# Kernel optimization log

Measured on AMD Instinct MI355X. Metric: run time of the kernel, lower is better.

## Reference

```python
import jax, jax.numpy as jnp
import numpy as np

B, P, F, H, NF, E, V, L = 128, 196, 2048, 512, 512, 512, 10000, 20
T = L - 1
EPS = 1e-5  # BatchNorm eps (eval mode, running_mean=0, running_var=1)


def setup_inputs() -> dict:
    key = jax.random.key(0)
    ks = jax.random.split(key, 16)

    def kaiming(k, out_d, in_d):
        return jax.random.normal(k, (out_d, in_d), jnp.float32) * np.float32(np.sqrt(2.0 / in_d))

    encoder_feat = jax.random.normal(ks[0], (B, P, F), jnp.float32)
    gt_captions = jax.random.randint(ks[1], (B, L), 0, V)
    # lengths in [2, L], sorted descending (torch code assumes this), max forced to L
    captions_len = jnp.sort(jax.random.randint(ks[2], (B,), 2, L + 1))[::-1].at[0].set(L)

    emb = jax.random.uniform(ks[3], (V, E), jnp.float32, -0.1, 0.1)
    Wfa = kaiming(ks[4], NF, F); bfa = jnp.zeros((NF,), jnp.float32)
    Wha = kaiming(ks[5], NF, H); bha = jnp.zeros((NF,), jnp.float32)
    Wv = kaiming(ks[6], 1, NF); bv = jnp.zeros((1,), jnp.float32)
    Wh0 = kaiming(ks[7], H, F); bh0 = jnp.zeros((H,), jnp.float32)
    Wc0 = kaiming(ks[8], H, F); bc0 = jnp.zeros((H,), jnp.float32)
    gamma_h = jnp.ones((H,), jnp.float32); beta_h = jnp.zeros((H,), jnp.float32)
    gamma_c = jnp.ones((H,), jnp.float32); beta_c = jnp.zeros((H,), jnp.float32)
    Wfb = kaiming(ks[9], F, H); bfb = jnp.zeros((F,), jnp.float32)
    s = np.float32(1.0 / np.sqrt(H))  # torch LSTMCell default init range
    Wih = jax.random.uniform(ks[10], (4 * H, E + F), jnp.float32, -s, s)
    Whh = jax.random.uniform(ks[11], (4 * H, H), jnp.float32, -s, s)
    bih = jax.random.uniform(ks[12], (4 * H,), jnp.float32, -s, s)
    bhh = jax.random.uniform(ks[13], (4 * H,), jnp.float32, -s, s)
    Wfc = kaiming(ks[14], V, H); bfc = jnp.zeros((V,), jnp.float32)

    return dict(encoder_feat=encoder_feat, emb=emb, Wfa=Wfa, bfa=bfa, Wha=Wha, bha=bha,
                Wv=Wv, bv=bv, Wh0=Wh0, bh0=bh0, Wc0=Wc0, bc0=bc0,
                gamma_h=gamma_h, beta_h=beta_h, gamma_c=gamma_c, beta_c=beta_c,
                Wfb=Wfb, bfb=bfb, Wih=Wih, Whh=Whh, bih=bih, bhh=bhh,
                Wfc=Wfc, bfc=bfc, gt_captions=gt_captions, captions_len=captions_len)


def reference(encoder_feat, emb, Wfa, bfa, Wha, bha, Wv, bv, Wh0, bh0, Wc0, bc0,
              gamma_h, beta_h, gamma_c, beta_c, Wfb, bfb, Wih, Whh, bih, bhh,
              Wfc, bfc, gt_captions, captions_len):
    # Eval-mode semantics: dropout = identity, weight-drop inactive,
    # BatchNorm1d uses default running stats (mean=0, var=1).
    def bn(x, g, b):
        return g * (x / jnp.sqrt(1.0 + EPS)) + b

    feat = encoder_feat.mean(axis=1)                       # [B, F]
    h = bn(jax.nn.sigmoid(feat @ Wh0.T + bh0), gamma_h, beta_h)
    c = bn(jax.nn.sigmoid(feat @ Wc0.T + bc0), gamma_c, beta_c)

    # attention key projection is h-independent: hoist out of the time loop
    feat_att = jnp.einsum('bpf,nf->bpn', encoder_feat, Wfa) + bfa  # [B, P, NF]
    emb_seq = emb[gt_captions]                                      # [B, L, E]

    # ragged batch handled by masking (equivalent to torch's [:batch_size_t] slicing)
    mask = (jnp.arange(T)[:, None] < (captions_len - 1)[None, :]).astype(encoder_feat.dtype)  # [T, B]
    xs = (jnp.swapaxes(emb_seq[:, :T], 0, 1), mask)

    def step(carry, xt):
        h, c = carry
        emb_t, m = xt                                      # [B, E], [B]
        att = jax.nn.relu(feat_att + (h @ Wha.T + bha)[:, None, :])
        e = jnp.einsum('bpn,n->bp', att, Wv[0]) + bv[0]    # [B, P]
        alpha = jax.nn.softmax(e, axis=1)
        context = jnp.einsum('bpf,bp->bf', encoder_feat, alpha)
        gate = jax.nn.sigmoid(h @ Wfb.T + bfb)             # [B, F]
        x = jnp.concatenate([emb_t, gate * context], axis=1)
        gates = x @ Wih.T + bih + h @ Whh.T + bhh          # [B, 4H]
        i, f, g, o = jnp.split(gates, 4, axis=1)
        c_new = jax.nn.sigmoid(f) * c + jax.nn.sigmoid(i) * jnp.tanh(g)
        h_new = jax.nn.sigmoid(o) * jnp.tanh(c_new)
        preds = h_new @ Wfc.T + bfc                        # [B, V]
        mf = m[:, None]
        return (h_new, c_new), (preds * mf, alpha * mf)

    _, (preds, alphas) = jax.lax.scan(step, (h, c), xs)
    predictions = jnp.swapaxes(preds, 0, 1)                # [B, T, V]
    alphas = jnp.swapaxes(alphas, 0, 1)                    # [B, T, P]
    return predictions, alphas
```

## Files before the change

kernel.cpp:

```cpp
#include <hip/hip_runtime.h>
#include <cstdint>
#include <cstddef>

#define B_  128
#define P_  196
#define F_  2048
#define H_  512
#define NF_ 512
#define E_  512
#define V_  10000
#define L_  20
#define T_  19
#define NPAD_ 10112

typedef short s8v __attribute__((ext_vector_type(8)));
typedef float f32x4 __attribute__((ext_vector_type(4)));
typedef unsigned short u16x8 __attribute__((ext_vector_type(8)));

__device__ __forceinline__ float sigf(float x) { return 1.0f / (1.0f + expf(-x)); }
__device__ __forceinline__ ushort f2b(float f) {
    unsigned u = __builtin_bit_cast(unsigned, f);
    u += 0x7fff + ((u >> 16) & 1);
    return (ushort)(u >> 16);
}
__device__ __forceinline__ float b2f(ushort h) {
    unsigned u = ((unsigned)h) << 16;
    return __builtin_bit_cast(float, u);
}

__global__ __launch_bounds__(256)
void cast_mat(const float* __restrict__ s, ushort* __restrict__ d,
              long long total, int cols, int sld, int srows) {
    long long i4 = ((long long)blockIdx.x * 256 + threadIdx.x) * 4;
    if (i4 >= total) return;
    int n = (int)(i4 / cols);
    int k = (int)(i4 - (long long)n * cols);
    float4 v = make_float4(0.f, 0.f, 0.f, 0.f);
    if (n < srows) v = *(const float4*)(s + (size_t)n * sld + k);
    ushort4 o;
    o.x = f2b(v.x); o.y = f2b(v.y); o.z = f2b(v.z); o.w = f2b(v.w);
    *(ushort4*)(d + i4) = o;
}

__global__ __launch_bounds__(256)
void cast_perm(const float* __restrict__ s, ushort* __restrict__ d,
               int cols, int sld) {
    int idx = blockIdx.x * 256 + threadIdx.x;
    int i4 = idx * 4;
    int n = i4 / cols;
    int k = i4 - n * cols;
    int r = (n & 3) * H_ + (n >> 2);
    float4 v = *(const float4*)(s + (size_t)r * sld + k);
    ushort4 o;
    o.x = f2b(v.x); o.y = f2b(v.y); o.z = f2b(v.z); o.w = f2b(v.w);
    *(ushort4*)(d + (size_t)n * cols + k) = o;
}

__global__ __launch_bounds__(256)
void build_bg(const float* __restrict__ bih, const float* __restrict__ bhh,
              float* __restrict__ bg) {
    int n = blockIdx.x * 256 + threadIdx.x;
    int r = (n & 3) * H_ + (n >> 2);
    bg[n] = bih[r] + bhh[r];
}

#define NCP_ (2560 + NPAD_)
__global__ __launch_bounds__(256)
void build_bcp(const float* __restrict__ bha, const float* __restrict__ bfb,
               const float* __restrict__ bfc, float* __restrict__ bcp) {
    int n = blockIdx.x * 256 + threadIdx.x;
    if (n >= NCP_) return;
    float v;
    if (n < 512) v = bha[n];
    else if (n < 2560) v = bfb[n - 512];
    else { int r = n - 2560; v = (r < V_) ? bfc[r] : 0.0f; }
    bcp[n] = v;
}

__global__ __launch_bounds__(256)
void mean_cast_kernel(const float* __restrict__ enc, ushort* __restrict__ encb,
                      float* __restrict__ feat) {
    int b = blockIdx.x >> 3;
    int f = ((blockIdx.x & 7) << 8) + threadIdx.x;
    const float* p = enc + (size_t)b * P_ * F_ + f;
    ushort* pb = encb + (size_t)b * P_ * F_ + f;
    float s = 0.0f;
    for (int q = 0; q < P_; q++) {
        float v = p[(size_t)q * F_];
        pb[(size_t)q * F_] = f2b(v);
        s += v;
    }
    feat[b * F_ + f] = s * (1.0f / 196.0f);
}

__global__ __launch_bounds__(256) void mean_kernel(const float* __restrict__ enc,
                                                   float* __restrict__ feat) {
    int b = blockIdx.x >> 3;
    int f = ((blockIdx.x & 7) << 8) + threadIdx.x;
    const float* p = enc + (size_t)b * P_ * F_ + f;
    float s = 0.0f;
    for (int q = 0; q < P_; q++) s += p[(size_t)q * F_];
    feat[b * F_ + f] = s * (1.0f / 196.0f);
}

__global__ __launch_bounds__(256) void gather_b(const float* __restrict__ emb,
                                                const int* __restrict__ gt,
                                                ushort* __restrict__ embx) {
    int idx = blockIdx.x * 256 + threadIdx.x;
    int i4 = idx * 4;
    int e = i4 & (E_ - 1);
    int bt = i4 >> 9;
    int b = bt / T_, t = bt - b * T_;
    int tok = gt[b * L_ + t];
    float4 v = *(const float4*)(emb + (size_t)tok * E_ + e);
    ushort4 o;
    o.x = f2b(v.x); o.y = f2b(v.y); o.z = f2b(v.z); o.w = f2b(v.w);
    *(ushort4*)(embx + i4) = o;
}

__global__ __launch_bounds__(256)
void gemm_biasb(const float* __restrict__ A, int lda,
                const float* __restrict__ W, int ldw,
                const float* __restrict__ bias,
                ushort* __restrict__ C, long long ldc,
                int M, int N, int K) {
    __shared__ float As[16][65];
    __shared__ float Ws[16][65];
    const int tid = threadIdx.x;
    const int m0 = blockIdx.y << 6;
    const int n0 = blockIdx.x << 6;
    const int row = tid >> 2;
    const int kq  = (tid & 3) << 2;
    const int ty = tid >> 4, tx = tid & 15;
    float acc[4][4] = {};
    for (int k0 = 0; k0 < K; k0 += 16) {
        float4 av = make_float4(0.f, 0.f, 0.f, 0.f);
        float4 wv = make_float4(0.f, 0.f, 0.f, 0.f);
        int m = m0 + row;
        if (m < M) av = *(const float4*)(A + (size_t)m * lda + k0 + kq);
        int n = n0 + row;
        if (n < N) wv = *(const float4*)(W + (size_t)n * ldw + k0 + kq);
        __syncthreads();
        As[kq + 0][row] = av.x; As[kq + 1][row] = av.y;
        As[kq + 2][row] = av.z; As[kq + 3][row] = av.w;
        Ws[kq + 0][row] = wv.x; Ws[kq + 1][row] = wv.y;
        Ws[kq + 2][row] = wv.z; Ws[kq + 3][row] = wv.w;
        __syncthreads();
#pragma unroll
        for (int k = 0; k < 16; k++) {
            float a[4], w[4];
#pragma unroll
            for (int i = 0; i < 4; i++) a[i] = As[k][(ty << 2) + i];
#pragma unroll
            for (int j = 0; j < 4; j++) w[j] = Ws[k][(tx << 2) + j];
#pragma unroll
            for (int i = 0; i < 4; i++)
#pragma unroll
                for (int j = 0; j < 4; j++)
                    acc[i][j] = fmaf(a[i], w[j], acc[i][j]);
        }
    }
#pragma unroll
    for (int i = 0; i < 4; i++) {
        int m = m0 + (ty << 2) + i;
        if (m >= M) continue;
#pragma unroll
        for (int j = 0; j < 4; j++) {
            int n = n0 + (tx << 2) + j;
            if (n >= N) continue;
            C[(size_t)m * ldc + n] = f2b(acc[i][j] + bias[n]);
        }
    }
}

enum { MEPI_NONE = 0, MEPI_BIAS = 1, MEPI_BIASB = 2, MEPI_PREDS = 3 };

__device__ __forceinline__ void stage_tile(const ushort* __restrict__ g, int ld,
                                           int row0, int k0, ushort* lds,
                                           int rows, int w, int l) {
    int nchunk = rows >> 4;
    for (int c = w; c < nchunk; c += 4) {
        int flat = c * 1024 + l * 16;
        int r = flat >> 6;
        int ce = (flat & 63) >> 1;
        const ushort* gp = g + (size_t)(row0 + r) * ld + (k0 + ce);
        __builtin_amdgcn_global_load_lds(
            (const __attribute__((address_space(1))) void*)gp,
            (__attribute__((address_space(3))) void*)(lds + c * 512),
            16, 0, 0);
    }
}

template <int BM, int EPI, int DUAL, int SWZ = 0>
__global__ __launch_bounds__(256)
void mfma_gemm(const ushort* __restrict__ A1, int lda1,
               const ushort* __restrict__ W1, int ldw1, int K1,
               const ushort* __restrict__ A2, int lda2,
               const ushort* __restrict__ W2, int ldw2, int K2,
               const float* __restrict__ bias, void* __restrict__ Cout, long long ldc,
               void* __restrict__ Cout2,
               int M, int N,
               const int* __restrict__ clen, int tcur) {
    __shared__ ushort As[BM * 32];
    __shared__ ushort Bs[128 * 32];
    const int tid = threadIdx.x;
    const int w = tid >> 6, l = tid & 63;
    const int wr = w >> 1, wc = w & 1;
    constexpr int WM = BM / 2;
    constexpr int AF = WM / 16;
    int bx = blockIdx.x, by = blockIdx.y;
    if (SWZ) {
        const int gx = gridDim.x;
        const int nwg = gx * gridDim.y;
        const int fid = by * gx + bx;
        const int q = nwg >> 3, r = nwg & 7;
        const int xcd = fid & 7, idx = fid >> 3;
        const int nf = (xcd < r ? xcd * (q + 1)
                                : r * (q + 1) + (xcd - r) * q) + idx;
        bx = nf % gx; by = nf / gx;
    }
    const int m0 = by * BM;
    const int n0 = bx * 128;
    const int lrow = l & 15, lk8 = (l >> 4) * 8;
    const int kz = blockIdx.z, nzz = gridDim.z;

    f32x4 acc[AF][4] = {};

    for (int pass = 0; pass < 1 + DUAL; pass++) {
        const ushort* A = pass ? A2 : A1;
        const ushort* W = pass ? W2 : W1;
        const int lda = pass ? lda2 : lda1;
        const int ldw = pass ? ldw2 : ldw1;
        const int K  = pass ? K2 : K1;
        const int chunk = K / nzz;
        const int kbeg = kz * chunk;
        const int kend = kbeg + chunk;
        for (int k0 = kbeg; k0 < kend; k0 += 32) {
            __syncthreads();
            stage_tile(A, lda, m0, k0, As, BM, w, l);
            stage_tile(W, ldw, n0, k0, Bs, 128, w, l);
            __syncthreads();
            s8v af[AF], bf[4];
#pragma unroll
            for (int i = 0; i < AF; i++)
                af[i] = *(const s8v*)(As + (wr * WM + i * 16 + lrow) * 32 + lk8);
#pragma unroll
            for (int j = 0; j < 4; j++)
                bf[j] = *(const s8v*)(Bs + (wc * 64 + j * 16 + lrow) * 32 + lk8);
#pragma unroll
            for (int i = 0; i < AF; i++)
#pragma unroll
                for (int j = 0; j < 4; j++)
                    acc[i][j] = __builtin_amdgcn_mfma_f32_16x16x32_bf16(
                        af[i], bf[j], acc[i][j], 0, 0, 0);
        }
    }

    float* Cz = (float*)Cout + (size_t)kz * (size_t)M * ldc;
#pragma unroll
    for (int i = 0; i < AF; i++) {
        int rb = m0 + wr * WM + i * 16 + (l >> 4) * 4;
#pragma unroll
        for (int j = 0; j < 4; j++) {
            int n = n0 + wc * 64 + j * 16 + (l & 15);
            if (n >= N) continue;
#pragma unroll
            for (int r = 0; r < 4; r++) {
                int m = rb + r;
                float v = acc[i][j][r];
                if (EPI == MEPI_NONE) {
                    Cz[(size_t)m * ldc + n] = v;
                } else if (EPI == MEPI_BIAS) {
                    ((float*)Cout)[(size_t)m * ldc + n] = v + bias[n];
                } else if (EPI == MEPI_BIASB) {
                    ((ushort*)Cout)[(size_t)m * ldc + n] = f2b(v + bias[n]);
                } else if (EPI == MEPI_PREDS) {
                    if (n < V_) {
                        int bb = m & (B_ - 1);
                        int tt = m >> 7;
                        float mk = (tt < clen[bb] - 1) ? 1.0f : 0.0f;
                        ((float*)Cout)[((size_t)bb * T_ + tt) * (size_t)V_ + n] =
                            (v + bias[n]) * mk;
                    }
                }
            }
        }
    }
}

__global__ __launch_bounds__(256)
void h0c0_final(const float* __restrict__ part,
                const float* __restrict__ b0,
                const float* __restrict__ g0,
                const float* __restrict__ bt0,
                float* __restrict__ cbuf, ushort* __restrict__ hb) {
    int idx = blockIdx.x * 256 + threadIdx.x;
    int b = idx >> 9, j = idx & 511;
    const float rbn = 1.0f / sqrtf(1.0f + 1e-5f);
    float sh = b0[j], sc = b0[j + 512];
    for (int z = 0; z < 4; z++) {
        sh += part[((size_t)z * B_ + b) * 1024 + j];
        sc += part[((size_t)z * B_ + b) * 1024 + j + 512];
    }
    float hv = g0[j] * (sigf(sh) * rbn) + bt0[j];
    float cv = g0[j + 512] * (sigf(sc) * rbn) + bt0[j + 512];
    cbuf[idx] = cv;
    hb[idx] = f2b(hv);
}

template <int BF>
__global__ __launch_bounds__(256)
void attn_ctx(const void* __restrict__ encv, const ushort* __restrict__ fa,
              const float* __restrict__ combo, const float* __restrict__ Wv,
              float* __restrict__ alphas_out, const int* __restrict__ clen,
              ushort* __restrict__ gctxb, int t) {
    int b = blockIdx.x >> 1;
    int half = blockIdx.x & 1;
    int tid = threadIdx.x;
    int w = tid >> 6, l = tid & 63;
    __shared__ float eS[256];
    __shared__ float red[256];
    __shared__ float pc[128 * 8];
    const float* hap = combo + (size_t)b * 2560;
    float ha8[8], wv8[8];
#pragma unroll
    for (int i = 0; i < 8; i++) { ha8[i] = hap[l * 8 + i]; wv8[i] = Wv[l * 8 + i]; }
    eS[tid] = -1e30f;
    __syncthreads();
    const ushort* fab = fa + (size_t)b * P_ * NF_;
    for (int p = w; p < P_; p += 4) {
        const ushort* fp = fab + (size_t)p * NF_ + l * 8;
        ushort4 u0 = *(const ushort4*)fp;
        ushort4 u1 = *(const ushort4*)(fp + 4);
        float s = 0.0f, v;
        v = b2f(u0.x) + ha8[0]; v = v > 0.f ? v : 0.f; s = fmaf(v, wv8[0], s);
        v = b2f(u0.y) + ha8[1]; v = v > 0.f ? v : 0.f; s = fmaf(v, wv8[1], s);
        v = b2f(u0.z) + ha8[2]; v = v > 0.f ? v : 0.f; s = fmaf(v, wv8[2], s);
        v = b2f(u0.w) + ha8[3]; v = v > 0.f ? v : 0.f; s = fmaf(v, wv8[3], s);
        v = b2f(u1.x) + ha8[4]; v = v > 0.f ? v : 0.f; s = fmaf(v, wv8[4], s);
        v = b2f(u1.y) + ha8[5]; v = v > 0.f ? v : 0.f; s = fmaf(v, wv8[5], s);
        v = b2f(u1.z) + ha8[6]; v = v > 0.f ? v : 0.f; s = fmaf(v, wv8[6], s);
        v = b2f(u1.w) + ha8[7]; v = v > 0.f ? v : 0.f; s = fmaf(v, wv8[7], s);
#pragma unroll
        for (int off = 32; off > 0; off >>= 1) s += __shfl_down(s, off, 64);
        if (l == 0) eS[p] = s;
    }
    __syncthreads();
    float ev = eS[tid];
    red[tid] = ev;
    __syncthreads();
    for (int s = 128; s > 0; s >>= 1) {
        if (tid < s) red[tid] = fmaxf(red[tid], red[tid + s]);
        __syncthreads();
    }
    float mx = red[0];
    __syncthreads();
    float ex = expf(ev - mx);
    red[tid] = ex;
    __syncthreads();
    for (int s = 128; s > 0; s >>= 1) {
        if (tid < s) red[tid] += red[tid + s];
        __syncthreads();
    }
    float inv = 1.0f / red[0];
    float a = ex * inv;
    __syncthreads();
    eS[tid] = a;
    if (half == 0 && tid < P_) {
        float m = (t < clen[b] - 1) ? 1.0f : 0.0f;
        alphas_out[((size_t)b * T_ + t) * P_ + tid] = a * m;
    }
    __syncthreads();

    int tl = tid & 127;
    int pr = tid >> 7;
    int pp0 = pr * 98;
    int f0 = (half << 10) + tl * 8;
    float s[8] = {};
    if (BF) {
        const ushort* ep = (const ushort*)encv + (size_t)b * P_ * F_ +
                           (size_t)pp0 * F_ + f0;
        for (int p = 0; p < 98; p++) {
            u16x8 u = *(const u16x8*)(ep + (size_t)p * F_);
            float al = eS[pp0 + p];
#pragma unroll
            for (int i = 0; i < 8; i++) s[i] = fmaf(al, b2f(u[i]), s[i]);
        }
    } else {
        const float* ep = (const float*)encv + (size_t)b * P_ * F_ +
                          (size_t)pp0 * F_ + f0;
        for (int p = 0; p < 98; p++) {
            float4 u0 = *(const float4*)(ep + (size_t)p * F_);
            float4 u1 = *(const float4*)(ep + (size_t)p * F_ + 4);
            float al = eS[pp0 + p];
            s[0] = fmaf(al, u0.x, s[0]); s[1] = fmaf(al, u0.y, s[1]);
            s[2] = fmaf(al, u0.z, s[2]); s[3] = fmaf(al, u0.w, s[3]);
            s[4] = fmaf(al, u1.x, s[4]); s[5] = fmaf(al, u1.y, s[5]);
            s[6] = fmaf(al, u1.z, s[6]); s[7] = fmaf(al, u1.w, s[7]);
        }
    }
    if (pr) {
#pragma unroll
        for (int i = 0; i < 8; i++) pc[tl * 8 + i] = s[i];
    }
    __syncthreads();
    if (!pr) {
        const float* gp = combo + (size_t)b * 2560 + 512 + f0;
        float4 ga = *(const float4*)gp;
        float4 gb = *(const float4*)(gp + 4);
        float gv[8] = {ga.x, ga.y, ga.z, ga.w, gb.x, gb.y, gb.z, gb.w};
        ushort o[8];
#pragma unroll
        for (int i = 0; i < 8; i++)
            o[i] = f2b(sigf(gv[i]) * (s[i] + pc[tl * 8 + i]));
        *(u16x8*)(gctxb + (size_t)b * F_ + f0) = *(u16x8*)o;
    }
}

__global__ __launch_bounds__(256)
void lstm_perm(const float* __restrict__ gatesP,
               const float* __restrict__ embprojP,
               const float* __restrict__ bg,
               float* __restrict__ cbuf, ushort* __restrict__ hout, int t) {
    int idx = blockIdx.x * 256 + threadIdx.x;
    int b = idx >> 9, j = idx & (H_ - 1);
    int n0 = j * 4;
    float4 g = *(const float4*)(embprojP + ((size_t)b * T_ + t) * 2048 + n0);
    float4 bgv = *(const float4*)(bg + n0);
    g.x += bgv.x; g.y += bgv.y; g.z += bgv.z; g.w += bgv.w;
#pragma unroll
    for (int z = 0; z < 4; z++) {
        float4 p = *(const float4*)(gatesP + ((size_t)z * B_ + b) * 2048 + n0);
        g.x += p.x; g.y += p.y; g.z += p.z; g.w += p.w;
    }
    float cn = sigf(g.y) * cbuf[idx] + sigf(g.x) * tanhf(g.z);
    float hn = sigf(g.w) * tanhf(cn);
    cbuf[idx] = cn;
    hout[idx] = f2b(hn);
}

extern "C" void kernel_launch(void* const* d_in, const int* in_sizes, int n_in,
                              void* d_out, int out_size, void* d_ws, size_t ws_size,
                              hipStream_t stream) {
    const float* enc = (const float*)d_in[0];
    const float* emb = (const float*)d_in[1];
    const float* Wfa = (const float*)d_in[2];
    const float* bfa = (const float*)d_in[3];
    const float* Wha = (const float*)d_in[4];
    const float* bha = (const float*)d_in[5];
    const float* Wv  = (const float*)d_in[6];
    const float* Wh0 = (const float*)d_in[8];
    const float* bh0 = (const float*)d_in[9];
    const float* Wc0 = (const float*)d_in[10];
    const float* bc0 = (const float*)d_in[11];
    const float* gh  = (const float*)d_in[12];
    const float* bth = (const float*)d_in[13];
    const float* gc  = (const float*)d_in[14];
    const float* btc = (const float*)d_in[15];
    const float* Wfb = (const float*)d_in[16];
    const float* bfb = (const float*)d_in[17];
    const float* Wih = (const float*)d_in[18];
    const float* Whh = (const float*)d_in[19];
    const float* bih = (const float*)d_in[20];
    const float* bhh = (const float*)d_in[21];
    const float* Wfc = (const float*)d_in[22];
    const float* bfc = (const float*)d_in[23];
    const int* gt   = (const int*)d_in[24];
    const int* clen = (const int*)d_in[25];

    float* out_pred  = (float*)d_out;
    float* out_alpha = out_pred + (size_t)B_ * T_ * V_;

    char* wp = (char*)d_ws;
    auto alloc = [&](size_t bytes) {
        char* p = wp;
        wp += (bytes + 255) & ~(size_t)255;
        return p;
    };
    float*  feat     = (float*)alloc((size_t)B_ * F_ * 4);
    float*  cbuf     = (float*)alloc((size_t)B_ * H_ * 4);
    float*  combo    = (float*)alloc((size_t)B_ * 2560 * 4);
    float*  embprojP = (float*)alloc((size_t)B_ * T_ * 2048 * 4);
    float*  gatesP   = (float*)alloc((size_t)4 * B_ * 2048 * 4);
    float*  hcpart   = (float*)alloc((size_t)4 * B_ * 1024 * 4);
    float*  bcp      = (float*)alloc((size_t)NCP_ * 4);
    float*  bg       = (float*)alloc(2048 * 4);
    float*  b0comb   = (float*)alloc(1024 * 4);
    float*  g0comb   = (float*)alloc(1024 * 4);
    float*  bt0comb  = (float*)alloc(1024 * 4);
    ushort* hall     = (ushort*)alloc((size_t)(T_ + 1) * B_ * H_ * 2);
    ushort* gctxb    = (ushort*)alloc((size_t)B_ * F_ * 2);
    ushort* embxb    = (ushort*)alloc((size_t)B_ * T_ * E_ * 2);
    ushort* fattb    = (ushort*)alloc((size_t)B_ * P_ * NF_ * 2);
    ushort* featb    = (ushort*)alloc((size_t)B_ * F_ * 2);
    ushort* Wfab     = (ushort*)alloc((size_t)NF_ * F_ * 2);
    ushort* WihEbP   = (ushort*)alloc((size_t)2048 * E_ * 2);
    ushort* WihFbP   = (ushort*)alloc((size_t)2048 * F_ * 2);
    ushort* WhhbP    = (ushort*)alloc((size_t)2048 * H_ * 2);
    ushort* Wcp      = (ushort*)alloc((size_t)NCP_ * H_ * 2);
    ushort* W0comb   = (ushort*)alloc((size_t)1024 * F_ * 2);
    ushort* encb     = (ushort*)alloc((size_t)B_ * P_ * F_ * 2);
    const bool big = ((size_t)(wp - (char*)d_ws) <= ws_size);

    auto castM = [&](const float* s, ushort* d, long long rows, int cols, int sld, int srows) {
        long long total = rows * (long long)cols;
        cast_mat<<<(int)((total + 1023) / 1024), 256, 0, stream>>>(s, d, total, cols, sld, srows);
    };

    castM(Wfa, Wfab, NF_, F_, F_, NF_);
    cast_perm<<<(2048 * E_) / 1024, 256, 0, stream>>>(Wih, WihEbP, E_, E_ + F_);
    cast_perm<<<(2048 * F_) / 1024, 256, 0, stream>>>(Wih + E_, WihFbP, F_, E_ + F_);
    cast_perm<<<(2048 * H_) / 1024, 256, 0, stream>>>(Whh, WhhbP, H_, H_);
    castM(Wha, Wcp, NF_, H_, H_, NF_);
    castM(Wfb, Wcp + (size_t)512 * H_, F_, H_, H_, F_);
    castM(Wfc, Wcp + (size_t)2560 * H_, NPAD_, H_, H_, V_);
    castM(Wh0, W0comb, H_, F_, F_, H_);
    castM(Wc0, W0comb + (size_t)H_ * F_, H_, F_, F_, H_);
    build_bg<<<2048 / 256, 256, 0, stream>>>(bih, bhh, bg);
    build_bcp<<<(NCP_ + 255) / 256, 256, 0, stream>>>(bha, bfb, bfc, bcp);
    hipMemcpyAsync(b0comb, bh0, H_ * 4, hipMemcpyDeviceToDevice, stream);
    hipMemcpyAsync(b0comb + H_, bc0, H_ * 4, hipMemcpyDeviceToDevice, stream);
    hipMemcpyAsync(g0comb, gh, H_ * 4, hipMemcpyDeviceToDevice, stream);
    hipMemcpyAsync(g0comb + H_, gc, H_ * 4, hipMemcpyDeviceToDevice, stream);
    hipMemcpyAsync(bt0comb, bth, H_ * 4, hipMemcpyDeviceToDevice, stream);
    hipMemcpyAsync(bt0comb + H_, btc, H_ * 4, hipMemcpyDeviceToDevice, stream);

    if (big) mean_cast_kernel<<<B_ * 8, 256, 0, stream>>>(enc, encb, feat);
    else     mean_kernel<<<B_ * 8, 256, 0, stream>>>(enc, feat);
    castM(feat, featb, B_, F_, F_, B_);
    mfma_gemm<32, MEPI_NONE, 0><<<dim3(1024 / 128, B_ / 32, 4), 256, 0, stream>>>(
        featb, F_, W0comb, F_, F_, nullptr, 0, nullptr, 0, 0,
        nullptr, hcpart, 1024, nullptr, B_, 1024, nullptr, 0);
    h0c0_final<<<(B_ * H_) / 256, 256, 0, stream>>>(hcpart, b0comb, g0comb, bt0comb, cbuf, hall);
    gather_b<<<(B_ * T_ * E_) / 1024, 256, 0, stream>>>(emb, gt, embxb);

    if (big) {
        mfma_gemm<128, MEPI_BIASB, 0, 1><<<dim3(NF_ / 128, (B_ * P_) / 128, 1), 256, 0, stream>>>(
            encb, F_, Wfab, F_, F_, nullptr, 0, nullptr, 0, 0,
            bfa, fattb, NF_, nullptr, B_ * P_, NF_, nullptr, 0);
    } else {
        gemm_biasb<<<dim3(NF_ / 64, (B_ * P_) / 64), 256, 0, stream>>>(
            enc, F_, Wfa, F_, bfa, fattb, NF_, B_ * P_, NF_, F_);
    }
    mfma_gemm<128, MEPI_NONE, 0><<<dim3(2048 / 128, (B_ * T_) / 128, 1), 256, 0, stream>>>(
        embxb, E_, WihEbP, E_, E_, nullptr, 0, nullptr, 0, 0,
        nullptr, embprojP, 2048, nullptr, B_ * T_, 2048, nullptr, 0);

    mfma_gemm<32, MEPI_BIAS, 0><<<dim3(2560 / 128, B_ / 32, 1), 256, 0, stream>>>(
        hall, H_, Wcp, H_, H_, nullptr, 0, nullptr, 0, 0,
        bcp, combo, 2560, nullptr, B_, 2560, nullptr, 0);

    for (int t = 0; t < T_; t++) {
        ushort* hin  = hall + (size_t)t * B_ * H_;
        ushort* hout = hall + (size_t)(t + 1) * B_ * H_;
        if (big) attn_ctx<1><<<B_ * 2, 256, 0, stream>>>(encb, fattb, combo, Wv,
                                                         out_alpha, clen, gctxb, t);
        else     attn_ctx<0><<<B_ * 2, 256, 0, stream>>>(enc, fattb, combo, Wv,
                                                         out_alpha, clen, gctxb, t);
        mfma_gemm<32, MEPI_NONE, 1><<<dim3(2048 / 128, B_ / 32, 4), 256, 0, stream>>>(
            gctxb, F_, WihFbP, F_, F_, hin, H_, WhhbP, H_, H_,
            nullptr, gatesP, 2048, nullptr, B_, 2048, nullptr, 0);
        lstm_perm<<<(B_ * H_) / 256, 256, 0, stream>>>(
            gatesP, embprojP, bg, cbuf, hout, t);
        mfma_gemm<32, MEPI_BIAS, 0><<<dim3(2560 / 128, B_ / 32, 1), 256, 0, stream>>>(
            hout, H_, Wcp, H_, H_, nullptr, 0, nullptr, 0, 0,
            bcp, combo, 2560, nullptr, B_, 2560, nullptr, 0);
    }

    mfma_gemm<128, MEPI_PREDS, 0, 1><<<dim3(NPAD_ / 128, (B_ * T_) / 128, 1), 256, 0, stream>>>(
        hall + (size_t)B_ * H_, H_, Wcp + (size_t)2560 * H_, H_, H_,
        nullptr, 0, nullptr, 0, 0,
        bcp + 2560, out_pred, V_, nullptr, B_ * T_, NPAD_, clen, 0);
}
```

Baseline: 1.989 ms.

## Skip finished sequences in the recurrent loop using caption lengths

Blocks in the attention, gate GEMM, LSTM cell and combo GEMM kernels now exit early when every row they own has passed its caption length, so masked timesteps are not computed. To keep the outputs correct, the hidden-state history and alpha output buffers are zeroed up front. Since lengths are sorted descending, whole 32-row tiles drop out at later steps. The cost is two extra zero-fill launches and a per-block check of the length array.

New measurement: 1.918 ms. 3.6% less time.

```diff
diff --git a/kernel.cpp b/kernel.cpp
--- a/kernel.cpp
+++ b/kernel.cpp
@@ -26,6 +26,12 @@
 __device__ __forceinline__ float b2f(ushort h) {
     unsigned u = ((unsigned)h) << 16;
     return __builtin_bit_cast(float, u);
+}
+
+__global__ __launch_bounds__(256)
+void zero_buf(float4* __restrict__ p, int n16) {
+    int i = blockIdx.x * 256 + threadIdx.x;
+    if (i < n16) p[i] = make_float4(0.f, 0.f, 0.f, 0.f);
 }
 
 __global__ __launch_bounds__(256)
@@ -191,7 +197,7 @@
     }
 }
 
-template <int BM, int EPI, int DUAL, int SWZ = 0>
+template <int BM, int EPI, int DUAL, int SWZ = 0, int MSK = 0>
 __global__ __launch_bounds__(256)
 void mfma_gemm(const ushort* __restrict__ A1, int lda1,
                const ushort* __restrict__ W1, int ldw1, int K1,
@@ -219,6 +225,10 @@
                                 : r * (q + 1) + (xcd - r) * q) + idx;
         bx = nf % gx; by = nf / gx;
     }
+    if (MSK) {
+        int cl = clen[by * BM + (l & (BM - 1))];
+        if (!__any(tcur < cl - 1)) return;
+    }
     const int m0 = by * BM;
     const int n0 = bx * 128;
     const int lrow = l & 15, lk8 = (l >> 4) * 8;
@@ -315,6 +325,7 @@
               float* __restrict__ alphas_out, const int* __restrict__ clen,
               ushort* __restrict__ gctxb, int t) {
     int b = blockIdx.x >> 1;
+    if (t >= clen[b] - 1) return;
     int half = blockIdx.x & 1;
     int tid = threadIdx.x;
     int w = tid >> 6, l = tid & 63;
@@ -367,8 +378,7 @@
     __syncthreads();
     eS[tid] = a;
     if (half == 0 && tid < P_) {
-        float m = (t < clen[b] - 1) ? 1.0f : 0.0f;
-        alphas_out[((size_t)b * T_ + t) * P_ + tid] = a * m;
+        alphas_out[((size_t)b * T_ + t) * P_ + tid] = a;
     }
     __syncthreads();
 
@@ -421,9 +431,11 @@
 void lstm_perm(const float* __restrict__ gatesP,
                const float* __restrict__ embprojP,
                const float* __restrict__ bg,
+               const int* __restrict__ clen,
                float* __restrict__ cbuf, ushort* __restrict__ hout, int t) {
     int idx = blockIdx.x * 256 + threadIdx.x;
     int b = idx >> 9, j = idx & (H_ - 1);
+    if (t >= clen[b] - 1) return;
     int n0 = j * 4;
     float4 g = *(const float4*)(embprojP + ((size_t)b * T_ + t) * 2048 + n0);
     float4 bgv = *(const float4*)(bg + n0);
@@ -507,6 +519,13 @@
         cast_mat<<<(int)((total + 1023) / 1024), 256, 0, stream>>>(s, d, total, cols, sld, srows);
     };
 
+    {
+        int n16h = (int)(((size_t)(T_ + 1) * B_ * H_ * 2) / 16);
+        zero_buf<<<(n16h + 255) / 256, 256, 0, stream>>>((float4*)hall, n16h);
+        int n16a = (int)(((size_t)B_ * T_ * P_ * 4) / 16);
+        zero_buf<<<(n16a + 255) / 256, 256, 0, stream>>>((float4*)out_alpha, n16a);
+    }
+
     castM(Wfa, Wfab, NF_, F_, F_, NF_);
     cast_perm<<<(2048 * E_) / 1024, 256, 0, stream>>>(Wih, WihEbP, E_, E_ + F_);
     cast_perm<<<(2048 * F_) / 1024, 256, 0, stream>>>(Wih + E_, WihFbP, F_, E_ + F_);
@@ -557,14 +576,14 @@
                                                          out_alpha, clen, gctxb, t);
         else     attn_ctx<0><<<B_ * 2, 256, 0, stream>>>(enc, fattb, combo, Wv,
                                                          out_alpha, clen, gctxb, t);
-        mfma_gemm<32, MEPI_NONE, 1><<<dim3(2048 / 128, B_ / 32, 4), 256, 0, stream>>>(
+        mfma_gemm<32, MEPI_NONE, 1, 0, 1><<<dim3(2048 / 128, B_ / 32, 4), 256, 0, stream>>>(
             gctxb, F_, WihFbP, F_, F_, hin, H_, WhhbP, H_, H_,
-            nullptr, gatesP, 2048, nullptr, B_, 2048, nullptr, 0);
+            nullptr, gatesP, 2048, nullptr, B_, 2048, clen, t);
         lstm_perm<<<(B_ * H_) / 256, 256, 0, stream>>>(
-            gatesP, embprojP, bg, cbuf, hout, t);
-        mfma_gemm<32, MEPI_BIAS, 0><<<dim3(2560 / 128, B_ / 32, 1), 256, 0, stream>>>(
+            gatesP, embprojP, bg, clen, cbuf, hout, t);
+        mfma_gemm<32, MEPI_BIAS, 0, 0, 1><<<dim3(2560 / 128, B_ / 32, 1), 256, 0, stream>>>(
             hout, H_, Wcp, H_, H_, nullptr, 0, nullptr, 0, 0,
-            bcp, combo, 2560, nullptr, B_, 2560, nullptr, 0);
+            bcp, combo, 2560, nullptr, B_, 2560, clen, t + 1);
     }
 
     mfma_gemm<128, MEPI_PREDS, 0, 1><<<dim3(NPAD_ / 128, (B_ * T_) / 128, 1), 256, 0, stream>>>(
```
